# Kernel optimization log

Hardware: AMD Instinct MI355X
Metric: run time of the kernel (lower is better)

## Reference

```python
import jax, jax.numpy as jnp
import numpy as np

B, S, DIM = 2, 2048, 2048
N_HEADS, N_KV_HEADS, HEAD_DIM = 16, 4, 128
ROPE_THETA = 10000.0
N_REP = N_HEADS // N_KV_HEADS


def make_freq_cis(seq_len, head_dim, theta):
    # (seq_len, head_dim//2, 2, 2) rotation matrices [[cos,-sin],[sin,cos]]
    freqs = 1.0 / (theta ** (np.arange(0, head_dim, 2, dtype=np.float32) / head_dim))
    t = np.arange(seq_len, dtype=np.float32)
    ang = np.outer(t, freqs)  # [S, head_dim//2]
    cos, sin = np.cos(ang), np.sin(ang)
    row0 = np.stack([cos, -sin], axis=-1)
    row1 = np.stack([sin, cos], axis=-1)
    return jnp.asarray(np.stack([row0, row1], axis=-2))  # [S, hd/2, 2, 2]


def setup_inputs() -> dict:
    key = jax.random.key(0)
    ks = jax.random.split(key, 5)
    std = DIM ** -0.5
    x = jax.random.normal(ks[0], (B, S, DIM), dtype=jnp.float32)
    wq = jax.random.normal(ks[1], (N_HEADS * HEAD_DIM, DIM), dtype=jnp.float32) * std
    wk = jax.random.normal(ks[2], (N_KV_HEADS * HEAD_DIM, DIM), dtype=jnp.float32) * std
    wv = jax.random.normal(ks[3], (N_KV_HEADS * HEAD_DIM, DIM), dtype=jnp.float32) * std
    wo = jax.random.normal(ks[4], (DIM, N_HEADS * HEAD_DIM), dtype=jnp.float32) * std
    freq_cis = make_freq_cis(S, HEAD_DIM, ROPE_THETA)
    return {"x": x, "freq_cis": freq_cis, "wq": wq, "wk": wk, "wv": wv, "wo": wo}


def apply_rotary(xh, fc):
    # xh: [B,S,H,hd]; fc: [S, hd/2, 2, 2]
    b, s, h, hd = xh.shape
    xr = xh.reshape(b, s, h, hd // 2, 2)
    out = jnp.einsum('bshdj,sdij->bshdi', xr, fc)
    return out.reshape(b, s, h, hd)


def attention_fwd(x, freq_cis, wq, wk, wv, wo):
    b, s, _ = x.shape
    xq = (x @ wq.T).reshape(b, s, N_HEADS, HEAD_DIM)
    xk = (x @ wk.T).reshape(b, s, N_KV_HEADS, HEAD_DIM)
    xv = (x @ wv.T).reshape(b, s, N_KV_HEADS, HEAD_DIM)
    xq = apply_rotary(xq, freq_cis[:s])
    xk = apply_rotary(xk, freq_cis[:s])
    # GQA repeat_kv (repeat_interleave along head dim)
    xk = jnp.repeat(xk, N_REP, axis=2)
    xv = jnp.repeat(xv, N_REP, axis=2)
    scale = HEAD_DIM ** -0.5
    scores = jnp.einsum('bqhd,bkhd->bhqk', xq, xk) * scale
    causal = jnp.tril(jnp.ones((s, s), dtype=bool))
    scores = jnp.where(causal[None, None], scores, jnp.float32(-1e30))
    probs = jax.nn.softmax(scores, axis=-1)
    out = jnp.einsum('bhqk,bkhd->bqhd', probs, xv).reshape(b, s, N_HEADS * HEAD_DIM)
    return out @ wo.T


def reference(x, freq_cis, wq, wk, wv, wo):
    return attention_fwd(x, freq_cis, wq, wk, wv, wo)
```

## Files before the change

### kernel.cpp

```cpp
#include <hip/hip_runtime.h>

#define S_LEN 2048
#define N_B 2
#define N_H 16
#define N_KVH 4
#define HD 128
#define LDQ 2048
#define LDK 1024

typedef __bf16 bf16x8 __attribute__((ext_vector_type(8)));
typedef float f32x4 __attribute__((ext_vector_type(4)));
typedef float f32x16 __attribute__((ext_vector_type(16)));
typedef int v2i __attribute__((ext_vector_type(2)));

__device__ __forceinline__ float bf2f(unsigned short u){
  unsigned int x = ((unsigned int)u) << 16; float f;
  __builtin_memcpy(&f, &x, 4); return f;
}
__device__ __forceinline__ unsigned short f2bf(float f){
  unsigned int x; __builtin_memcpy(&x, &f, 4);
  unsigned int r = x + 0x7fff + ((x >> 16) & 1);
  return (unsigned short)(r >> 16);
}
__device__ __forceinline__ unsigned int cvt_pk_bf16(float lo, float hi){
  unsigned int u;
  asm("v_cvt_pk_bf16_f32 %0, %1, %2" : "=v"(u) : "v"(lo), "v"(hi));
  return u;
}
__device__ __forceinline__ void gload16(const void* g, void* l){
  __builtin_amdgcn_global_load_lds((const __attribute__((address_space(1))) void*)g,
                                   (__attribute__((address_space(3))) void*)l, 16, 0, 0);
}

__global__ void cast_bf16(const float* __restrict__ in, unsigned short* __restrict__ out, int n8){
  int i = blockIdx.x * 256 + threadIdx.x;
  if (i >= n8) return;
  const float4* p = (const float4*)in + (size_t)i * 2;
  float4 a = p[0], b = p[1];
  uint4 o;
  o.x = (unsigned)f2bf(a.x) | ((unsigned)f2bf(a.y) << 16);
  o.y = (unsigned)f2bf(a.z) | ((unsigned)f2bf(a.w) << 16);
  o.z = (unsigned)f2bf(b.x) | ((unsigned)f2bf(b.y) << 16);
  o.w = (unsigned)f2bf(b.z) | ((unsigned)f2bf(b.w) << 16);
  ((uint4*)out)[i] = o;
}

__global__ void rope_kernel(unsigned short* __restrict__ X, const float* __restrict__ FC,
                            int cpr_log2, int ld_log2, int n8){
  int i = blockIdx.x * 256 + threadIdx.x;
  if (i >= n8) return;
  int row = i >> cpr_log2;
  int col = (i & ((1 << cpr_log2) - 1)) << 3;
  size_t idx = ((size_t)row << ld_log2) + col;
  int s = row & (S_LEN - 1);
  int d = col & (HD - 1);
  uint4 v = *(const uint4*)(X + idx);
  unsigned short* pv = (unsigned short*)&v;
  const float4* f4 = (const float4*)FC + ((size_t)s * 64 + (d >> 1));
  uint4 ov; unsigned short* po = (unsigned short*)&ov;
#pragma unroll
  for (int p = 0; p < 4; p++){
    float4 f = f4[p];
    float e = bf2f(pv[2*p]), o = bf2f(pv[2*p+1]);
    po[2*p]   = f2bf(f.x * e + f.y * o);
    po[2*p+1] = f2bf(f.z * e + f.w * o);
  }
  *(uint4*)(X + idx) = ov;
}

__global__ void transpose_v(const unsigned short* __restrict__ V, unsigned short* __restrict__ Vt, int ld){
  __shared__ unsigned short tile[32][33];
  int t = threadIdx.x;
  int s0 = blockIdx.x * 32;
  int c0 = blockIdx.y * 32;
  int r = t >> 3, cg = (t & 7) * 4;
  uint2 in2 = *(const uint2*)(V + (size_t)(s0 + r) * ld + c0 + cg);
  unsigned short* pi = (unsigned short*)&in2;
  tile[r][cg+0] = pi[0]; tile[r][cg+1] = pi[1]; tile[r][cg+2] = pi[2]; tile[r][cg+3] = pi[3];
  __syncthreads();
  int b = s0 >> 11, sl = s0 & (S_LEN - 1);
  int kvh = c0 >> 7, dd0 = c0 & (HD - 1);
  int dd = t >> 3, sg = (t & 7) * 4;
  uint2 o2; unsigned short* po = (unsigned short*)&o2;
  po[0] = tile[sg+0][dd]; po[1] = tile[sg+1][dd]; po[2] = tile[sg+2][dd]; po[3] = tile[sg+3][dd];
  *(uint2*)(Vt + (size_t)((b * N_KVH + kvh) * HD + dd0 + dd) * S_LEN + sl + sg) = o2;
}

__device__ __forceinline__ void storeC(float* C, size_t idx, float v){ C[idx] = v; }
__device__ __forceinline__ void storeC(unsigned short* C, size_t idx, float v){ C[idx] = f2bf(v); }

template <typename OutT>
__global__ __launch_bounds__(256, 2) void gemm_nt(const unsigned short* __restrict__ A,
                                                  const unsigned short* __restrict__ Bm,
                                                  OutT* __restrict__ C,
                                                  int M, int N, int K, int nbn){
  extern __shared__ char smem[];
  char* sA = smem; char* sB = smem + 16384;
  int bid = blockIdx.x;
  bid = (bid & 7) * (gridDim.x >> 3) + (bid >> 3);
  int bn = bid % nbn, bm = bid / nbn;
  int row0 = bm * 128, col0 = bn * 128;
  int t = threadIdx.x; int w = t >> 6, l = t & 63;
  int lr = l & 15, lg = l >> 4;
  int srow = t >> 3;
  int sg = (t & 7) ^ (srow & 7);
  const unsigned short* agp = A + (size_t)(row0 + srow) * K + sg * 8;
  const unsigned short* bgp = Bm + (size_t)(col0 + srow) * K + sg * 8;
  int wr = w >> 1, wc = w & 1;
  f32x4 acc[4][4] = {};
  for (int k0 = 0; k0 < K; k0 += 64){
    __syncthreads();
#pragma unroll
    for (int i = 0; i < 4; i++){
      gload16(agp + (size_t)i * 32 * K + k0, sA + i * 4096 + w * 1024);
      gload16(bgp + (size_t)i * 32 * K + k0, sB + i * 4096 + w * 1024);
    }
    __syncthreads();
#pragma unroll
    for (int kk = 0; kk < 2; kk++){
      bf16x8 af[4], bfv[4];
#pragma unroll
      for (int m = 0; m < 4; m++){
        int row = wr * 64 + m * 16 + lr;
        int kg = kk * 4 + lg;
        af[m] = *(const bf16x8*)(sA + row * 128 + ((kg ^ (row & 7)) << 4));
      }
#pragma unroll
      for (int n = 0; n < 4; n++){
        int row = wc * 64 + n * 16 + lr;
        int kg = kk * 4 + lg;
        bfv[n] = *(const bf16x8*)(sB + row * 128 + ((kg ^ (row & 7)) << 4));
      }
#pragma unroll
      for (int m = 0; m < 4; m++)
#pragma unroll
        for (int n = 0; n < 4; n++)
          acc[m][n] = __builtin_amdgcn_mfma_f32_16x16x32_bf16(af[m], bfv[n], acc[m][n], 0, 0, 0);
    }
  }
#pragma unroll
  for (int m = 0; m < 4; m++)
#pragma unroll
    for (int n = 0; n < 4; n++)
#pragma unroll
      for (int r = 0; r < 4; r++){
        int rr = row0 + wr * 64 + m * 16 + lg * 4 + r;
        int cc = col0 + wc * 64 + n * 16 + lr;
        storeC(C, (size_t)rr * N + cc, acc[m][n][r]);
      }
}

template <typename OutT>
__global__ __launch_bounds__(512, 2) void gemm_tpl(const unsigned short* __restrict__ A,
                                                   const unsigned short* __restrict__ Bm,
                                                   OutT* __restrict__ C,
                                                   int M, int N, int K, int nbn){
  extern __shared__ char smem[];
  int bid = blockIdx.x;
  bid = (bid & 7) * (gridDim.x >> 3) + (bid >> 3);
  int bn = bid % nbn, bm = bid / nbn;
  int row0 = bm * 128, col0 = bn * 256;
  int t = threadIdx.x, w = t >> 6, l = t & 63;
  int lr = l & 15, lg = l >> 4;
  int wm = w >> 2, wn = w & 3;
  int srow = t >> 3;
  int sg = (t & 7) ^ (srow & 7);
  const unsigned short* agp = A + (size_t)(row0 + srow) * K + sg * 8;
  const unsigned short* bgp = Bm + (size_t)(col0 + srow) * K + sg * 8;
  int nk = K >> 6;
  f32x4 acc[4][4] = {};

#define TPL_STAGE(j, s) do {                                                   \
    char* base_ = smem + (s) * 49152;                                          \
    int k0_ = (j) << 6;                                                        \
    _Pragma("unroll")                                                          \
    for (int i_ = 0; i_ < 2; i_++)                                             \
      gload16(agp + (size_t)i_ * 64 * K + k0_, base_ + i_ * 8192 + w * 1024);  \
    _Pragma("unroll")                                                          \
    for (int i_ = 0; i_ < 4; i_++)                                             \
      gload16(bgp + (size_t)i_ * 64 * K + k0_, base_ + 16384 + i_ * 8192 + w * 1024); \
  } while(0)

  TPL_STAGE(0, 0);
  TPL_STAGE(1, 1);
  int slot = 0;
  for (int j = 0; j < nk; j++){
    if (j + 1 < nk) asm volatile("s_waitcnt vmcnt(6)" ::: "memory");
    else            asm volatile("s_waitcnt vmcnt(0)" ::: "memory");
    __builtin_amdgcn_s_barrier();
    asm volatile("" ::: "memory");
    char* sA = smem + slot * 49152;
    char* sB = sA + 16384;
    bf16x8 af[2][4], bf[2][4];
#pragma unroll
    for (int kk = 0; kk < 2; kk++){
#pragma unroll
      for (int m = 0; m < 4; m++){
        int row = wm * 64 + m * 16 + lr;
        int kg = kk * 4 + lg;
        af[kk][m] = *(const bf16x8*)(sA + row * 128 + ((kg ^ (row & 7)) << 4));
      }
#pragma unroll
      for (int n = 0; n < 4; n++){
        int row = wn * 64 + n * 16 + lr;
        int kg = kk * 4 + lg;
        bf[kk][n] = *(const bf16x8*)(sB + row * 128 + ((kg ^ (row & 7)) << 4));
      }
    }
    if (j + 2 < nk){
      int sn = slot + 2; if (sn >= 3) sn -= 3;
      TPL_STAGE(j + 2, sn);
    }
    __builtin_amdgcn_s_setprio(1);
#pragma unroll
    for (int kk = 0; kk < 2; kk++)
#pragma unroll
      for (int m = 0; m < 4; m++)
#pragma unroll
        for (int n = 0; n < 4; n++)
          acc[m][n] = __builtin_amdgcn_mfma_f32_16x16x32_bf16(af[kk][m], bf[kk][n], acc[m][n], 0, 0, 0);
    __builtin_amdgcn_s_setprio(0);
    slot++; if (slot == 3) slot = 0;
  }
#undef TPL_STAGE
#pragma unroll
  for (int m = 0; m < 4; m++)
#pragma unroll
    for (int n = 0; n < 4; n++)
#pragma unroll
      for (int r = 0; r < 4; r++){
        int rr = row0 + wm * 64 + m * 16 + lg * 4 + r;
        int cc = col0 + wn * 64 + n * 16 + lr;
        storeC(C, (size_t)rr * N + cc, acc[m][n][r]);
      }
}

__global__ __launch_bounds__(256, 2) void attn_fwd(const unsigned short* __restrict__ Q,
                                                   const unsigned short* __restrict__ Kb,
                                                   const unsigned short* __restrict__ Vt,
                                                   unsigned short* __restrict__ P0,
                                                   unsigned short* __restrict__ P1,
                                                   float2* __restrict__ ML){
  extern __shared__ char smem[];
  const float SOFT_C = 0.088388347648318447f * 1.4426950408889634f;
  const float THR_RAW = 62.0f;
  int bid = blockIdx.x;
  bid = ((bid & 7) << 6) | (bid >> 3);
  int slot = bid & 15, h = (bid >> 4) & 15, b = bid >> 8;
  int p = slot & 7, half = slot >> 3;
  int kvh = h >> 2;
  int t = threadIdx.x, w = t >> 6, l = t & 63;
  int lq = l & 31, lh = l >> 5;
  unsigned short* Pout = half ? P1 : P0;
  float2* mlb = ML + half * (N_B * S_LEN * N_H);

  int gA = (t & 15) ^ (t >> 4);
  const unsigned short* kgp = Kb + ((size_t)(b * S_LEN) + (t >> 4)) * LDK + kvh * HD + gA * 8;
  int gV = (t & 7) ^ ((t >> 3) & 7);
  const unsigned short* vgp = Vt + ((size_t)((b * N_KVH + kvh) * HD) + (t >> 3)) * S_LEN + gV * 8;

  for (int phase = 0; phase < 2; phase++){
    int qt = phase ? (15 - p) : p;
    int q_lane = qt * 128 + w * 32 + lq;
    const unsigned short* qbase = Q + ((size_t)(b * S_LEN + q_lane)) * LDQ + h * HD + lh * 8;
    bf16x8 qf[8];
#pragma unroll
    for (int ks = 0; ks < 8; ks++)
      qf[ks] = *(const bf16x8*)(qbase + ks * 16);

    f32x16 o_acc[4] = {};
    float m_run = -1e4f, l_run = 0.f;
    int t_begin = half ? (qt + 1) : 0;
    int t_end   = half ? (2 * qt + 2) : (qt + 1);

    int pk0 = t_begin * 64;
#pragma unroll
    for (int m = 0; m < 4; m++)
      gload16(kgp + (size_t)(pk0 + m * 16) * LDK, smem + m * 4096 + w * 1024);
#pragma unroll
    for (int i = 0; i < 4; i++)
      gload16(vgp + (size_t)i * 32 * S_LEN + pk0, smem + 16384 + i * 4096 + w * 1024);
    __syncthreads();

    int cur = 0;
    for (int tix = t_begin; tix < t_end; tix++){
      int k0 = tix * 64;
      char* sK = smem + (cur << 15);
      char* sV = sK + 16384;
      if (tix + 1 < t_end){
        char* nb = smem + ((cur ^ 1) << 15);
        int nk0 = k0 + 64;
#pragma unroll
        for (int m = 0; m < 4; m++)
          gload16(kgp + (size_t)(nk0 + m * 16) * LDK, nb + m * 4096 + w * 1024);
#pragma unroll
        for (int i = 0; i < 4; i++)
          gload16(vgp + (size_t)i * 32 * S_LEN + nk0, nb + 16384 + i * 4096 + w * 1024);
      }

      f32x16 sc[2] = {};
      __builtin_amdgcn_s_setprio(1);
#pragma unroll
      for (int ks = 0; ks < 8; ks++){
#pragma unroll
        for (int n = 0; n < 2; n++){
          int row = n * 32 + lq;
          int pg = (ks * 2 + lh) ^ (row & 15);
          bf16x8 kf = *(const bf16x8*)(sK + row * 256 + pg * 16);
          sc[n] = __builtin_amdgcn_mfma_f32_32x32x16_bf16(kf, qf[ks], sc[n], 0, 0, 0);
        }
      }
      __builtin_amdgcn_s_setprio(0);
      if (tix >= 2 * qt){
#pragma unroll
        for (int n = 0; n < 2; n++)
#pragma unroll
          for (int reg = 0; reg < 16; reg++){
            int kv = k0 + n * 32 + (reg & 3) + 8 * (reg >> 2) + 4 * lh;
            if (kv > q_lane) sc[n][reg] = -1e30f;
          }
      }
      float tmax = sc[0][0];
#pragma unroll
      for (int n = 0; n < 2; n++)
#pragma unroll
        for (int reg = 0; reg < 16; reg++) tmax = fmaxf(tmax, sc[n][reg]);
      tmax = fmaxf(tmax, __shfl_xor(tmax, 32));
      if (!__all(tmax - m_run <= THR_RAW)){
        float nm = fmaxf(m_run, tmax);
        float rs = exp2f((m_run - nm) * SOFT_C);
        m_run = nm;
        l_run *= rs;
#pragma unroll
        for (int n = 0; n < 4; n++)
#pragma unroll
          for (int j = 0; j < 16; j++) o_acc[n][j] *= rs;
      }
      float lsum = 0.f;
#pragma unroll
      for (int n = 0; n < 2; n++)
#pragma unroll
        for (int reg = 0; reg < 16; reg++){
          float pv = exp2f((sc[n][reg] - m_run) * SOFT_C);
          sc[n][reg] = pv;
          lsum += pv;
        }
      lsum += __shfl_xor(lsum, 32);
      l_run += lsum;

      bf16x8 pb[4];
#pragma unroll
      for (int ks = 0; ks < 4; ks++){
        int n = ks >> 1;
        int R0 = (2 * ks) & 3, R1 = (2 * ks + 1) & 3;
        unsigned int WA0 = cvt_pk_bf16(sc[n][4 * R0 + 0], sc[n][4 * R0 + 1]);
        unsigned int WA1 = cvt_pk_bf16(sc[n][4 * R0 + 2], sc[n][4 * R0 + 3]);
        unsigned int WB0 = cvt_pk_bf16(sc[n][4 * R1 + 0], sc[n][4 * R1 + 1]);
        unsigned int WB1 = cvt_pk_bf16(sc[n][4 * R1 + 2], sc[n][4 * R1 + 3]);
        v2i s0 = __builtin_amdgcn_permlane32_swap((int)WA0, (int)WB0, false, false);
        v2i s1 = __builtin_amdgcn_permlane32_swap((int)WA1, (int)WB1, false, false);
        unsigned int pu[4] = {(unsigned int)s0.x, (unsigned int)s1.x,
                              (unsigned int)s0.y, (unsigned int)s1.y};
        pb[ks] = *(bf16x8*)pu;
      }
      __builtin_amdgcn_s_setprio(1);
#pragma unroll
      for (int n = 0; n < 4; n++){
#pragma unroll
        for (int ks = 0; ks < 4; ks++){
          int row = n * 32 + lq;
          int pg = (ks * 2 + lh) ^ (row & 7);
          bf16x8 vf = *(const bf16x8*)(sV + row * 128 + pg * 16);
          o_acc[n] = __builtin_amdgcn_mfma_f32_32x32x16_bf16(vf, pb[ks], o_acc[n], 0, 0, 0);
        }
      }
      __builtin_amdgcn_s_setprio(0);
      __syncthreads();
      cur ^= 1;
    }
    unsigned short* ob = Pout + ((size_t)(b * S_LEN + q_lane)) * LDQ + h * HD + 4 * lh;
#pragma unroll
    for (int n = 0; n < 4; n++)
#pragma unroll
      for (int g = 0; g < 4; g++){
        unsigned int u0 = cvt_pk_bf16(o_acc[n][4 * g + 0], o_acc[n][4 * g + 1]);
        unsigned int u1 = cvt_pk_bf16(o_acc[n][4 * g + 2], o_acc[n][4 * g + 3]);
        uint2 o2; o2.x = u0; o2.y = u1;
        *(uint2*)(ob + n * 32 + g * 8) = o2;
      }
    if (lh == 0)
      mlb[(size_t)(b * S_LEN + q_lane) * N_H + h] = make_float2(m_run, l_run);
  }
}

__global__ void attn_merge(unsigned short* __restrict__ P0, const unsigned short* __restrict__ P1,
                           const float2* __restrict__ ML){
  const float SOFT_C = 0.088388347648318447f * 1.4426950408889634f;
  int tid = blockIdx.x * 256 + threadIdx.x;
  float2 a = ML[tid >> 4];
  float2 c = ML[(N_B * S_LEN * N_H) + (tid >> 4)];
  float m = fmaxf(a.x, c.x);
  float w0 = exp2f((a.x - m) * SOFT_C) * a.y;
  float w1 = exp2f((c.x - m) * SOFT_C) * c.y;
  float inv = 1.0f / (w0 + w1);
  float s0 = exp2f((a.x - m) * SOFT_C) * inv;
  float s1 = exp2f((c.x - m) * SOFT_C) * inv;
  uint4 u0 = *(const uint4*)(P0 + (size_t)tid * 8);
  uint4 u1 = *(const uint4*)(P1 + (size_t)tid * 8);
  unsigned short* q0 = (unsigned short*)&u0;
  unsigned short* q1 = (unsigned short*)&u1;
  uint4 o;
  unsigned int* po = (unsigned int*)&o;
#pragma unroll
  for (int j = 0; j < 4; j++){
    float lo = s0 * bf2f(q0[2*j])   + s1 * bf2f(q1[2*j]);
    float hi = s0 * bf2f(q0[2*j+1]) + s1 * bf2f(q1[2*j+1]);
    po[j] = cvt_pk_bf16(lo, hi);
  }
  *(uint4*)(P0 + (size_t)tid * 8) = o;
}

extern "C" void kernel_launch(void* const* d_in, const int* in_sizes, int n_in,
                              void* d_out, int out_size, void* d_ws, size_t ws_size,
                              hipStream_t stream) {
  const float* x  = (const float*)d_in[0];
  const float* fc = (const float*)d_in[1];
  const float* wq = (const float*)d_in[2];
  const float* wk = (const float*)d_in[3];
  const float* wv = (const float*)d_in[4];
  const float* wo = (const float*)d_in[5];
  float* out = (float*)d_out;

  char* ws = (char*)d_ws;
  unsigned short* xb  = (unsigned short*)(ws);
  unsigned short* wqb = (unsigned short*)(ws + 16777216);
  unsigned short* wkb = (unsigned short*)(ws + 25165824);
  unsigned short* wvb = (unsigned short*)(ws + 27262976);
  unsigned short* wob = (unsigned short*)(ws + 29360128);
  unsigned short* qb_ = (unsigned short*)(ws + 37748736);
  unsigned short* kvb = (unsigned short*)(ws + 54525952);
  unsigned short* vtb = (unsigned short*)(ws + 62914560);
  unsigned short* ab_ = (unsigned short*)(ws + 67108864);
  unsigned short* p1_ = xb;
  float2*         ml_ = (float2*)wqb;

  cast_bf16<<<4096, 256, 0, stream>>>(x,  xb,  1048576);
  cast_bf16<<<2048, 256, 0, stream>>>(wq, wqb, 524288);
  cast_bf16<<<512,  256, 0, stream>>>(wk, wkb, 131072);
  cast_bf16<<<512,  256, 0, stream>>>(wv, wvb, 131072);
  cast_bf16<<<2048, 256, 0, stream>>>(wo, wob, 524288);

  gemm_tpl<unsigned short><<<256, 512, 147456, stream>>>(xb, wqb, qb_, 4096, 2048, 2048, 8);
  gemm_nt<unsigned short><<<256, 256, 32768, stream>>>(xb, wkb, kvb, 4096, 1024, 2048, 8);

  rope_kernel<<<4096, 256, 0, stream>>>(qb_, fc, 8, 11, 1048576);
  rope_kernel<<<1024, 256, 0, stream>>>(kvb, fc, 6, 10, 262144);

  transpose_v<<<dim3(128, 16), 256, 0, stream>>>(kvb + 512, vtb, 1024);

  attn_fwd<<<512, 256, 65536, stream>>>(qb_, kvb, vtb, ab_, p1_, ml_);
  attn_merge<<<4096, 256, 0, stream>>>(ab_, p1_, ml_);

  gemm_tpl<float><<<256, 512, 147456, stream>>>(ab_, wob, out, 4096, 2048, 2048, 8);
}
```

Before: 213.5 us.

## Shrink attention tiles to 64 queries and 32 keys, fuse cast kernels

```diff
diff --git a/kernel.cpp b/kernel.cpp
--- a/kernel.cpp
+++ b/kernel.cpp
@@ -32,17 +32,26 @@
                                    (__attribute__((address_space(3))) void*)l, 16, 0, 0);
 }
 
-__global__ void cast_bf16(const float* __restrict__ in, unsigned short* __restrict__ out, int n8){
+__global__ void cast_all(const float* __restrict__ x,  const float* __restrict__ wq,
+                         const float* __restrict__ wk, const float* __restrict__ wv,
+                         const float* __restrict__ wo, unsigned short* __restrict__ xb,
+                         unsigned short* __restrict__ wqb, unsigned short* __restrict__ wkb,
+                         unsigned short* __restrict__ wvb, unsigned short* __restrict__ wob){
   int i = blockIdx.x * 256 + threadIdx.x;
-  if (i >= n8) return;
-  const float4* p = (const float4*)in + (size_t)i * 2;
+  const float* in; unsigned short* out; int j;
+  if (i < 1048576)      { in = x;  out = xb;  j = i; }
+  else if (i < 1572864) { in = wq; out = wqb; j = i - 1048576; }
+  else if (i < 1703936) { in = wk; out = wkb; j = i - 1572864; }
+  else if (i < 1835008) { in = wv; out = wvb; j = i - 1703936; }
+  else                  { in = wo; out = wob; j = i - 1835008; }
+  const float4* p = (const float4*)in + (size_t)j * 2;
   float4 a = p[0], b = p[1];
   uint4 o;
   o.x = (unsigned)f2bf(a.x) | ((unsigned)f2bf(a.y) << 16);
   o.y = (unsigned)f2bf(a.z) | ((unsigned)f2bf(a.w) << 16);
   o.z = (unsigned)f2bf(b.x) | ((unsigned)f2bf(b.y) << 16);
   o.w = (unsigned)f2bf(b.z) | ((unsigned)f2bf(b.w) << 16);
-  ((uint4*)out)[i] = o;
+  ((uint4*)out)[j] = o;
 }
 
 __global__ void rope_kernel(unsigned short* __restrict__ X, const float* __restrict__ FC,
@@ -235,7 +244,7 @@
       }
 }
 
-__global__ __launch_bounds__(256, 2) void attn_fwd(const unsigned short* __restrict__ Q,
+__global__ __launch_bounds__(128, 2) void attn_fwd(const unsigned short* __restrict__ Q,
                                                    const unsigned short* __restrict__ Kb,
                                                    const unsigned short* __restrict__ Vt,
                                                    unsigned short* __restrict__ P0,
@@ -245,23 +254,21 @@
   const float SOFT_C = 0.088388347648318447f * 1.4426950408889634f;
   const float THR_RAW = 62.0f;
   int bid = blockIdx.x;
-  bid = ((bid & 7) << 6) | (bid >> 3);
-  int slot = bid & 15, h = (bid >> 4) & 15, b = bid >> 8;
-  int p = slot & 7, half = slot >> 3;
+  bid = ((bid & 7) << 7) | (bid >> 3);
+  int slot = bid & 31, h = (bid >> 5) & 15, b = bid >> 9;
+  int p = slot & 15, half = slot >> 4;
   int kvh = h >> 2;
   int t = threadIdx.x, w = t >> 6, l = t & 63;
   int lq = l & 31, lh = l >> 5;
   unsigned short* Pout = half ? P1 : P0;
   float2* mlb = ML + half * (N_B * S_LEN * N_H);
 
-  int gA = (t & 15) ^ (t >> 4);
-  const unsigned short* kgp = Kb + ((size_t)(b * S_LEN) + (t >> 4)) * LDK + kvh * HD + gA * 8;
-  int gV = (t & 7) ^ ((t >> 3) & 7);
-  const unsigned short* vgp = Vt + ((size_t)((b * N_KVH + kvh) * HD) + (t >> 3)) * S_LEN + gV * 8;
+  const unsigned short* kgp = Kb + ((size_t)(b * S_LEN) + (t & 31)) * LDK + kvh * HD + (t >> 5) * 8;
+  const unsigned short* vgp = Vt + ((size_t)((b * N_KVH + kvh) * HD) + t) * S_LEN;
 
   for (int phase = 0; phase < 2; phase++){
-    int qt = phase ? (15 - p) : p;
-    int q_lane = qt * 128 + w * 32 + lq;
+    int qt = phase ? (31 - p) : p;
+    int q_lane = qt * 64 + w * 32 + lq;
     const unsigned short* qbase = Q + ((size_t)(b * S_LEN + q_lane)) * LDQ + h * HD + lh * 8;
     bf16x8 qf[8];
 #pragma unroll
@@ -273,58 +280,48 @@
     int t_begin = half ? (qt + 1) : 0;
     int t_end   = half ? (2 * qt + 2) : (qt + 1);
 
-    int pk0 = t_begin * 64;
-#pragma unroll
-    for (int m = 0; m < 4; m++)
-      gload16(kgp + (size_t)(pk0 + m * 16) * LDK, smem + m * 4096 + w * 1024);
-#pragma unroll
-    for (int i = 0; i < 4; i++)
-      gload16(vgp + (size_t)i * 32 * S_LEN + pk0, smem + 16384 + i * 4096 + w * 1024);
+    {
+      int k0 = t_begin * 32;
+#pragma unroll
+      for (int i = 0; i < 4; i++){
+        gload16(kgp + (size_t)k0 * LDK + i * 32, smem + i * 2048 + t * 16);
+        gload16(vgp + k0 + i * 8, smem + 8192 + i * 2048 + t * 16);
+      }
+    }
     __syncthreads();
 
     int cur = 0;
     for (int tix = t_begin; tix < t_end; tix++){
-      int k0 = tix * 64;
-      char* sK = smem + (cur << 15);
-      char* sV = sK + 16384;
+      int k0 = tix * 32;
+      char* kb = smem + (cur << 14);
       if (tix + 1 < t_end){
-        char* nb = smem + ((cur ^ 1) << 15);
-        int nk0 = k0 + 64;
-#pragma unroll
-        for (int m = 0; m < 4; m++)
-          gload16(kgp + (size_t)(nk0 + m * 16) * LDK, nb + m * 4096 + w * 1024);
-#pragma unroll
-        for (int i = 0; i < 4; i++)
-          gload16(vgp + (size_t)i * 32 * S_LEN + nk0, nb + 16384 + i * 4096 + w * 1024);
-      }
-
-      f32x16 sc[2] = {};
+        char* nb = smem + ((cur ^ 1) << 14);
+        int nk0 = k0 + 32;
+#pragma unroll
+        for (int i = 0; i < 4; i++){
+          gload16(kgp + (size_t)nk0 * LDK + i * 32, nb + i * 2048 + t * 16);
+          gload16(vgp + nk0 + i * 8, nb + 8192 + i * 2048 + t * 16);
+        }
+      }
+
+      f32x16 sc = {};
       __builtin_amdgcn_s_setprio(1);
 #pragma unroll
       for (int ks = 0; ks < 8; ks++){
-#pragma unroll
-        for (int n = 0; n < 2; n++){
-          int row = n * 32 + lq;
-          int pg = (ks * 2 + lh) ^ (row & 15);
-          bf16x8 kf = *(const bf16x8*)(sK + row * 256 + pg * 16);
-          sc[n] = __builtin_amdgcn_mfma_f32_32x32x16_bf16(kf, qf[ks], sc[n], 0, 0, 0);
-        }
+        bf16x8 kf = *(const bf16x8*)(kb + ks * 1024 + lh * 512 + lq * 16);
+        sc = __builtin_amdgcn_mfma_f32_32x32x16_bf16(kf, qf[ks], sc, 0, 0, 0);
       }
       __builtin_amdgcn_s_setprio(0);
       if (tix >= 2 * qt){
 #pragma unroll
-        for (int n = 0; n < 2; n++)
-#pragma unroll
-          for (int reg = 0; reg < 16; reg++){
-            int kv = k0 + n * 32 + (reg & 3) + 8 * (reg >> 2) + 4 * lh;
-            if (kv > q_lane) sc[n][reg] = -1e30f;
-          }
-      }
-      float tmax = sc[0][0];
-#pragma unroll
-      for (int n = 0; n < 2; n++)
-#pragma unroll
-        for (int reg = 0; reg < 16; reg++) tmax = fmaxf(tmax, sc[n][reg]);
+        for (int reg = 0; reg < 16; reg++){
+          int kv = k0 + (reg & 3) + 8 * (reg >> 2) + 4 * lh;
+          if (kv > q_lane) sc[reg] = -1e30f;
+        }
+      }
+      float tmax = sc[0];
+#pragma unroll
+      for (int reg = 1; reg < 16; reg++) tmax = fmaxf(tmax, sc[reg]);
       tmax = fmaxf(tmax, __shfl_xor(tmax, 32));
       if (!__all(tmax - m_run <= THR_RAW)){
         float nm = fmaxf(m_run, tmax);
@@ -338,25 +335,21 @@
       }
       float lsum = 0.f;
 #pragma unroll
-      for (int n = 0; n < 2; n++)
-#pragma unroll
-        for (int reg = 0; reg < 16; reg++){
-          float pv = exp2f((sc[n][reg] - m_run) * SOFT_C);
-          sc[n][reg] = pv;
-          lsum += pv;
-        }
+      for (int reg = 0; reg < 16; reg++){
+        float pv = exp2f((sc[reg] - m_run) * SOFT_C);
+        sc[reg] = pv;
+        lsum += pv;
+      }
       lsum += __shfl_xor(lsum, 32);
       l_run += lsum;
 
-      bf16x8 pb[4];
-#pragma unroll
-      for (int ks = 0; ks < 4; ks++){
-        int n = ks >> 1;
-        int R0 = (2 * ks) & 3, R1 = (2 * ks + 1) & 3;
-        unsigned int WA0 = cvt_pk_bf16(sc[n][4 * R0 + 0], sc[n][4 * R0 + 1]);
-        unsigned int WA1 = cvt_pk_bf16(sc[n][4 * R0 + 2], sc[n][4 * R0 + 3]);
-        unsigned int WB0 = cvt_pk_bf16(sc[n][4 * R1 + 0], sc[n][4 * R1 + 1]);
-        unsigned int WB1 = cvt_pk_bf16(sc[n][4 * R1 + 2], sc[n][4 * R1 + 3]);
+      bf16x8 pb[2];
+#pragma unroll
+      for (int ks = 0; ks < 2; ks++){
+        unsigned int WA0 = cvt_pk_bf16(sc[8*ks+0], sc[8*ks+1]);
+        unsigned int WA1 = cvt_pk_bf16(sc[8*ks+2], sc[8*ks+3]);
+        unsigned int WB0 = cvt_pk_bf16(sc[8*ks+4], sc[8*ks+5]);
+        unsigned int WB1 = cvt_pk_bf16(sc[8*ks+6], sc[8*ks+7]);
         v2i s0 = __builtin_amdgcn_permlane32_swap((int)WA0, (int)WB0, false, false);
         v2i s1 = __builtin_amdgcn_permlane32_swap((int)WA1, (int)WB1, false, false);
         unsigned int pu[4] = {(unsigned int)s0.x, (unsigned int)s1.x,
@@ -367,10 +360,8 @@
 #pragma unroll
       for (int n = 0; n < 4; n++){
 #pragma unroll
-        for (int ks = 0; ks < 4; ks++){
-          int row = n * 32 + lq;
-          int pg = (ks * 2 + lh) ^ (row & 7);
-          bf16x8 vf = *(const bf16x8*)(sV + row * 128 + pg * 16);
+        for (int ks = 0; ks < 2; ks++){
+          bf16x8 vf = *(const bf16x8*)(kb + 8192 + ks * 4096 + lh * 2048 + n * 512 + lq * 16);
           o_acc[n] = __builtin_amdgcn_mfma_f32_32x32x16_bf16(vf, pb[ks], o_acc[n], 0, 0, 0);
         }
       }
@@ -444,11 +435,7 @@
   unsigned short* p1_ = xb;
   float2*         ml_ = (float2*)wqb;
 
-  cast_bf16<<<4096, 256, 0, stream>>>(x,  xb,  1048576);
-  cast_bf16<<<2048, 256, 0, stream>>>(wq, wqb, 524288);
-  cast_bf16<<<512,  256, 0, stream>>>(wk, wkb, 131072);
-  cast_bf16<<<512,  256, 0, stream>>>(wv, wvb, 131072);
-  cast_bf16<<<2048, 256, 0, stream>>>(wo, wob, 524288);
+  cast_all<<<9216, 256, 0, stream>>>(x, wq, wk, wv, wo, xb, wqb, wkb, wvb, wob);
 
   gemm_tpl<unsigned short><<<256, 512, 147456, stream>>>(xb, wqb, qb_, 4096, 2048, 2048, 8);
   gemm_nt<unsigned short><<<256, 256, 32768, stream>>>(xb, wkb, kvb, 4096, 1024, 2048, 8);
@@ -458,7 +445,7 @@
 
   transpose_v<<<dim3(128, 16), 256, 0, stream>>>(kvb + 512, vtb, 1024);
 
-  attn_fwd<<<512, 256, 65536, stream>>>(qb_, kvb, vtb, ab_, p1_, ml_);
+  attn_fwd<<<1024, 128, 32768, stream>>>(qb_, kvb, vtb, ab_, p1_, ml_);
   attn_merge<<<4096, 256, 0, stream>>>(ab_, p1_, ml_);
 
   gemm_tpl<float><<<256, 512, 147456, stream>>>(ab_, wob, out, 4096, 2048, 2048, 8);
```

Result: slower. 230.6 us (+8.0%).
